# Kernel optimization log

Measured on AMD Instinct MI355X. Metric: run time of the kernel, lower is better.

Reference implementation:

```python
import jax, jax.numpy as jnp
import numpy as np

B, IN_DIM, H, OUT_DIM, T = 2048, 1024, 2048, 1024, 10


def setup_inputs() -> dict:
    key = jax.random.key(0)
    ks = jax.random.split(key, 16)
    s = lambda d: 1.0 / np.sqrt(d)
    inp = {
        "x": jax.random.normal(ks[0], (B, IN_DIM), jnp.float32),
        "z0": jax.random.normal(ks[1], (B, H), jnp.float32),
        "noise": jax.random.normal(ks[2], (T, B, H), jnp.float32),
        # input_embed: Linear(IN,H) -> SiLU -> Linear(H,H)
        "w1_in": jax.random.normal(ks[3], (IN_DIM, H), jnp.float32) * s(IN_DIM),
        "b1_in": jnp.zeros((H,), jnp.float32),
        "w2_in": jax.random.normal(ks[4], (H, H), jnp.float32) * s(H),
        "b2_in": jnp.zeros((H,), jnp.float32),
        # T blocks: Linear(2H,H) -> SiLU -> Linear(H,H), stacked over T
        "wA": jax.random.normal(ks[5], (T, 2 * H, H), jnp.float32) * s(2 * H),
        "bA": jnp.zeros((T, H), jnp.float32),
        "wB": jax.random.normal(ks[6], (T, H, H), jnp.float32) * s(H),
        "bB": jnp.zeros((T, H), jnp.float32),
        # classifier Linear(H, OUT)
        "wC": jax.random.normal(ks[7], (H, OUT_DIM), jnp.float32) * s(H),
        "bC": jnp.zeros((OUT_DIM,), jnp.float32),
    }
    return inp


def _forward(x, z0, noise, w1_in, b1_in, w2_in, b2_in, wA, bA, wB, bB, wC, bC):
    # input embedding
    h = jax.nn.silu(x @ w1_in + b1_in)
    x_embed = h @ w2_in + b2_in  # (B, H)

    alpha = jnp.linspace(0.99, 0.9, T).astype(x.dtype)          # (T,)
    noise_scale = jnp.sqrt(1.0 - alpha)                          # (T,)

    def step(z, per_t):
        wA_t, bA_t, wB_t, bB_t, n_t, a_t, ns_t = per_t
        u = jax.nn.silu(jnp.concatenate([z, x_embed], axis=-1) @ wA_t + bA_t)
        u = u @ wB_t + bB_t
        z_next = a_t * u + (1.0 - a_t) * z + ns_t * n_t
        return z_next, None

    z_final, _ = jax.lax.scan(step, z0, (wA, bA, wB, bB, noise, alpha, noise_scale))
    return z_final @ wC + bC  # (B, OUT_DIM)


def reference(x, z0, noise, w1_in, b1_in, w2_in, b2_in, wA, bA, wB, bB, wC, bC):
    return _forward(x, z0, noise, w1_in, b1_in, w2_in, b2_in, wA, bA, wB, bB, wC, bC)
```

## Files before the change

### kernel.cpp

```cpp
#include <hip/hip_runtime.h>
#include <math.h>

typedef _Float16 f16;
typedef _Float16 f16x4 __attribute__((ext_vector_type(4)));
typedef _Float16 f16x8 __attribute__((ext_vector_type(8)));
typedef float f32x4 __attribute__((ext_vector_type(4)));
typedef float fvec4 __attribute__((ext_vector_type(4)));

#define EP_SILU 0
#define EP_LIN  1
#define EP_ZUP  2
#define EP_OUT  3
#define EP_ADDP 4

struct TDesc {
  const float* W;
  f16* WT;
  long long sW, sWT;
  int R, C, nMat;
};

__device__ __forceinline__ void gll16(const void* g, void* l) {
  __builtin_amdgcn_global_load_lds((__attribute__((address_space(1))) void*)g,
                                   (__attribute__((address_space(3))) void*)l,
                                   16, 0, 0);
}

__device__ __forceinline__ void stage_tile(const f16* __restrict__ g, int ld,
                                           f16* ldsTile, int tid, int wid) {
#pragma unroll
  for (int p = 0; p < 2; ++p) {
    int row = p * 64 + (tid >> 2);
    int col = (tid & 3) * 8;
    gll16(g + (size_t)row * ld + col, ldsTile + p * 2048 + wid * 512);
  }
}

__device__ __forceinline__ void stage8(const f16* __restrict__ g, int ld,
                                       f16* ldsTile, int tid) {
  int row = tid >> 2, col = (tid & 3) * 8;
  gll16(g + (size_t)row * ld + col, ldsTile + tid * 8);
}

__device__ __forceinline__ void tpose_tile(const float* __restrict__ W,
                                           f16* __restrict__ WT, int R, int C,
                                           int r0, int c0, f16 (*t)[72],
                                           int tid) {
#pragma unroll
  for (int p = 0; p < 2; ++p) {
    int lin = p * 2048 + tid * 4;
    int r = lin >> 6, c4 = lin & 63;
    fvec4 v = *(const fvec4*)(W + (size_t)(r0 + r) * C + c0 + c4);
    t[c4 + 0][r] = (f16)v[0];
    t[c4 + 1][r] = (f16)v[1];
    t[c4 + 2][r] = (f16)v[2];
    t[c4 + 3][r] = (f16)v[3];
  }
  __syncthreads();
#pragma unroll
  for (int p = 0; p < 2; ++p) {
    int lin = p * 2048 + tid * 4;
    int c = lin >> 6, r4 = lin & 63;
    f16x4 h;
    h[0] = t[c][r4 + 0];
    h[1] = t[c][r4 + 1];
    h[2] = t[c][r4 + 2];
    h[3] = t[c][r4 + 3];
    *(f16x4*)(WT + (size_t)(c0 + c) * R + r0 + r4) = h;
  }
  __syncthreads();
}

__device__ void run_role(const TDesc d, int rid, int nr, f16 (*t)[72],
                         int tid) {
  if (d.nMat <= 0 || d.W == nullptr) return;
  int tR = d.R >> 6, tC = d.C >> 6;
  int tpm = tR * tC, tot = tpm * d.nMat;
  for (int i = rid; i < tot; i += nr) {
    int m = i / tpm, rem = i - m * tpm;
    int r0 = (rem % tR) << 6, c0 = (rem / tR) << 6;
    tpose_tile(d.W + (size_t)m * d.sW, d.WT + (size_t)m * d.sWT, d.R, d.C, r0,
               c0, t, tid);
  }
}

template <int EP>
__global__ void __launch_bounds__(512)
gemm8(const f16* __restrict__ A, int lda, const f16* __restrict__ BT, int ldb,
      int K, int N, int gx, int nbGemm, const float* __restrict__ bias,
      const f16* __restrict__ addP, f16* __restrict__ outH,
      float* __restrict__ outF, const f16* __restrict__ zOld,
      const float* __restrict__ noise, float aT, float nsT, TDesc dA,
      TDesc dB) {
  __shared__ __align__(16) char smem[65536];
  const int tid = threadIdx.x;
  const int bid = blockIdx.x;

  if (bid >= nbGemm) {
    int rid = bid - nbGemm, nr = (int)gridDim.x - nbGemm;
    f16(*t)[72] = reinterpret_cast<f16(*)[72]>(smem);
    run_role(dA, rid, nr, t, tid);
    run_role(dB, rid, nr, t, tid);
    return;
  }

  const int cpx = nbGemm >> 3;
  const int swz = (bid & 7) * cpx + (bid >> 3);
  const int by = swz / gx, bx = swz % gx;
  const int m0 = by * 128, n0 = bx * 128;

  const int lane = tid & 63, wid = tid >> 6;
  const int q = wid & 3, h = wid >> 2;
  const int wr = q >> 1, wc = q & 1;
  const int lr = lane & 15, kg = lane >> 4;

  f16* base = (f16*)smem;
  f32x4 acc[4][4] = {};

  const int nkp = K >> 6;
  auto stageAB = [&](int kp, int slot) {
    int k0 = kp << 6;
    f16* s = base + slot * 16384;
    stage8(A + (size_t)m0 * lda + k0, lda, s, tid);
    stage8(A + (size_t)m0 * lda + k0 + 32, lda, s + 4096, tid);
    stage8(BT + (size_t)n0 * ldb + k0, ldb, s + 8192, tid);
    stage8(BT + (size_t)n0 * ldb + k0 + 32, ldb, s + 12288, tid);
  };

  stageAB(0, 0);
  __syncthreads();
  int cur = 0;
  for (int kp = 0; kp < nkp; ++kp) {
    if (kp + 1 < nkp) stageAB(kp + 1, cur ^ 1);
    const f16* LA = base + cur * 16384 + h * 4096;
    const f16* LB = base + cur * 16384 + 8192 + h * 4096;
    f16x8 a[4], b[4];
#pragma unroll
    for (int m = 0; m < 4; ++m)
      a[m] = *(const f16x8*)(LA + ((wr * 64 + m * 16 + lr) * 32 + kg * 8));
#pragma unroll
    for (int n = 0; n < 4; ++n)
      b[n] = *(const f16x8*)(LB + ((wc * 64 + n * 16 + lr) * 32 + kg * 8));
#pragma unroll
    for (int m = 0; m < 4; ++m)
#pragma unroll
      for (int n = 0; n < 4; ++n)
        acc[m][n] = __builtin_amdgcn_mfma_f32_16x16x32_f16(a[m], b[n],
                                                           acc[m][n], 0, 0, 0);
    __syncthreads();
    cur ^= 1;
  }

  float* red = (float*)smem;
  if (h == 1) {
#pragma unroll
    for (int m = 0; m < 4; ++m)
#pragma unroll
      for (int n = 0; n < 4; ++n) {
        int row = wr * 64 + m * 16 + kg * 4;
        int col = wc * 64 + n * 16 + lr;
        *(f32x4*)&red[(size_t)col * 128 + row] = acc[m][n];
      }
  }
  __syncthreads();
  if (h != 0) return;

  float bcol[4];
  if constexpr (EP != EP_ADDP) {
#pragma unroll
    for (int n = 0; n < 4; ++n) bcol[n] = bias[n0 + wc * 64 + n * 16 + lr];
  }

#pragma unroll
  for (int m = 0; m < 4; ++m) {
    int rowb = m0 + wr * 64 + m * 16 + kg * 4;
    int rowl = wr * 64 + m * 16 + kg * 4;
#pragma unroll
    for (int n = 0; n < 4; ++n) {
      int col = n0 + wc * 64 + n * 16 + lr;
      int coll = wc * 64 + n * 16 + lr;
      f32x4 osum = acc[m][n] + *(const f32x4*)&red[(size_t)coll * 128 + rowl];
#pragma unroll
      for (int r = 0; r < 4; ++r) {
        size_t idx = (size_t)(rowb + r) * N + col;
        float v = osum[r];
        if constexpr (EP == EP_ADDP) v += (float)addP[idx];
        else v += bcol[n];
        if constexpr (EP == EP_SILU || EP == EP_ADDP) {
          v = v / (1.0f + __expf(-v));
          outH[idx] = (f16)v;
        } else if constexpr (EP == EP_LIN) {
          outH[idx] = (f16)v;
        } else if constexpr (EP == EP_OUT) {
          outF[idx] = v;
        } else {
          float zn = aT * v + (1.0f - aT) * (float)zOld[idx] + nsT * noise[idx];
          outH[idx] = (f16)zn;
        }
      }
    }
  }
}

template <int EP>
__global__ void __launch_bounds__(256)
gemm_bt(const f16* __restrict__ A0, const f16* __restrict__ A1, int Ksplit,
        int lda, const f16* __restrict__ BT, int ldb, long long sBT, int K,
        int N, int gx, const float* __restrict__ bias, long long sBias,
        f16* __restrict__ outH, float* __restrict__ outF, long long sOut,
        const float* __restrict__ zOld, const float* __restrict__ noise,
        float aT, float nsT) {
  __shared__ __align__(16) f16 lds[2][2][128 * 32];
  const int tid = threadIdx.x;
  const int z = blockIdx.z;
  const f16* BTz = BT + (size_t)z * sBT;
  f16* outHz = outH + (size_t)z * sOut;
  float* outFz = outF ? outF + (size_t)z * sOut : nullptr;

  const int lane = tid & 63, wid = tid >> 6;
  const int wr = wid >> 1, wc = wid & 1;
  const int lr = lane & 15, kg = lane >> 4;
  const int by = blockIdx.x / gx, bx = blockIdx.x - by * gx;
  const int m0 = by * 128, n0 = bx * 128;

  f32x4 acc[4][4] = {};
  const int nk = K >> 5;
  auto stageAB = [&](int kt, int buf) {
    int k0 = kt << 5;
    const f16* Abase = (k0 < Ksplit)
                           ? (A0 + (size_t)m0 * lda + k0)
                           : (A1 + (size_t)m0 * lda + (k0 - Ksplit));
    stage_tile(Abase, lda, &lds[buf][0][0], tid, wid);
    stage_tile(BTz + (size_t)n0 * ldb + k0, ldb, &lds[buf][1][0], tid, wid);
  };

  stageAB(0, 0);
  __syncthreads();
  int cur = 0;
  for (int kt = 0; kt < nk; ++kt) {
    if (kt + 1 < nk) stageAB(kt + 1, cur ^ 1);
    const f16* LA = &lds[cur][0][0];
    const f16* LB = &lds[cur][1][0];
    f16x8 a[4], b[4];
#pragma unroll
    for (int m = 0; m < 4; ++m)
      a[m] = *(const f16x8*)(LA + ((wr * 64 + m * 16 + lr) * 32 + kg * 8));
#pragma unroll
    for (int n = 0; n < 4; ++n)
      b[n] = *(const f16x8*)(LB + ((wc * 64 + n * 16 + lr) * 32 + kg * 8));
#pragma unroll
    for (int m = 0; m < 4; ++m)
#pragma unroll
      for (int n = 0; n < 4; ++n)
        acc[m][n] = __builtin_amdgcn_mfma_f32_16x16x32_f16(a[m], b[n],
                                                           acc[m][n], 0, 0, 0);
    __syncthreads();
    cur ^= 1;
  }

  float bcol[4];
  const float* biasz = bias + (size_t)z * sBias;
#pragma unroll
  for (int n = 0; n < 4; ++n) bcol[n] = biasz[n0 + wc * 64 + n * 16 + lr];

#pragma unroll
  for (int m = 0; m < 4; ++m) {
    int rowb = m0 + wr * 64 + m * 16 + kg * 4;
#pragma unroll
    for (int n = 0; n < 4; ++n) {
      int col = n0 + wc * 64 + n * 16 + lr;
#pragma unroll
      for (int r = 0; r < 4; ++r) {
        size_t idx = (size_t)(rowb + r) * N + col;
        float v = acc[m][n][r] + bcol[n];
        if constexpr (EP == EP_SILU) {
          v = v / (1.0f + __expf(-v));
          outHz[idx] = (f16)v;
        } else if constexpr (EP == EP_LIN) {
          outHz[idx] = (f16)v;
        } else if constexpr (EP == EP_OUT) {
          outFz[idx] = v;
        } else {
          float zn = aT * v + (1.0f - aT) * zOld[idx] + nsT * noise[idx];
          outFz[idx] = zn;
          outHz[idx] = (f16)zn;
        }
      }
    }
  }
}

__global__ void __launch_bounds__(512) tconv_role(TDesc d) {
  __shared__ __align__(16) f16 t[64][72];
  run_role(d, blockIdx.x, gridDim.x, t, threadIdx.x);
}

__global__ void __launch_bounds__(256)
cvt4(const float* __restrict__ in, f16* __restrict__ outp, int n4) {
  int i = blockIdx.x * 256 + threadIdx.x;
  if (i >= n4) return;
  fvec4 v = *(const fvec4*)(in + (size_t)i * 4);
  f16x4 h;
  h[0] = (f16)v[0];
  h[1] = (f16)v[1];
  h[2] = (f16)v[2];
  h[3] = (f16)v[3];
  *(f16x4*)(outp + (size_t)i * 4) = h;
}

__global__ void __launch_bounds__(256)
zinit4(const float* __restrict__ z0, float* __restrict__ z32,
       f16* __restrict__ z16, int n4) {
  int i = blockIdx.x * 256 + threadIdx.x;
  if (i >= n4) return;
  fvec4 v = *(const fvec4*)(z0 + (size_t)i * 4);
  *(fvec4*)(z32 + (size_t)i * 4) = v;
  f16x4 h;
  h[0] = (f16)v[0];
  h[1] = (f16)v[1];
  h[2] = (f16)v[2];
  h[3] = (f16)v[3];
  *(f16x4*)(z16 + (size_t)i * 4) = h;
}

extern "C" void kernel_launch(void* const* d_in, const int* in_sizes, int n_in,
                              void* d_out, int out_size, void* d_ws,
                              size_t ws_size, hipStream_t stream) {
  const int B = 2048, IN = 1024, H = 2048, OUT = 1024, T = 10;
  const float* x = (const float*)d_in[0];
  const float* z0 = (const float*)d_in[1];
  const float* noise = (const float*)d_in[2];
  const float* w1 = (const float*)d_in[3];
  const float* b1 = (const float*)d_in[4];
  const float* w2 = (const float*)d_in[5];
  const float* b2 = (const float*)d_in[6];
  const float* wA = (const float*)d_in[7];
  const float* bA = (const float*)d_in[8];
  const float* wB = (const float*)d_in[9];
  const float* bB = (const float*)d_in[10];
  const float* wC = (const float*)d_in[11];
  const float* bC = (const float*)d_in[12];
  float* out = (float*)d_out;

  char* ws = (char*)d_ws;
  size_t off = 0;
  auto alloc = [&](size_t bytes) {
    void* p = ws + off;
    off += (bytes + 255) & ~(size_t)255;
    return p;
  };
  TDesc none = {nullptr, nullptr, 0, 0, 0, 0, 0};

  const size_t FAST_NEED = 273000000ull;
  if (ws_size >= FAST_NEED) {
    f16* x16 = (f16*)alloc((size_t)B * IN * 2);
    f16* h16 = (f16*)alloc((size_t)B * H * 2);
    f16* xe16 = (f16*)alloc((size_t)B * H * 2);
    f16* z16 = (f16*)alloc((size_t)B * H * 2);
    f16* u16 = (f16*)alloc((size_t)B * H * 2);
    f16* p16 = (f16*)alloc((size_t)T * B * H * 2);
    f16* w1T = (f16*)alloc((size_t)IN * H * 2);
    f16* w2T = (f16*)alloc((size_t)H * H * 2);
    f16* wCT = (f16*)alloc((size_t)H * OUT * 2);
    f16* wAbotT = (f16*)alloc((size_t)T * H * H * 2);
    f16* wAtopT[2] = {(f16*)alloc((size_t)H * H * 2),
                      (f16*)alloc((size_t)H * H * 2)};
    f16* wBT2[2] = {(f16*)alloc((size_t)H * H * 2),
                    (f16*)alloc((size_t)H * H * 2)};

    cvt4<<<B * IN / 4 / 256, 256, 0, stream>>>(x, x16, B * IN / 4);
    cvt4<<<B * H / 4 / 256, 256, 0, stream>>>(z0, z16, B * H / 4);
    tconv_role<<<512, 512, 0, stream>>>(TDesc{w1, w1T, 0, 0, IN, H, 1});

    gemm8<EP_SILU><<<512, 512, 0, stream>>>(
        x16, IN, w1T, IN, IN, H, 16, 256, b1, nullptr, h16, nullptr, nullptr,
        nullptr, 0.f, 0.f, TDesc{w2, w2T, 0, 0, H, H, 1},
        TDesc{wA + (size_t)H * H, wAbotT, (long long)2 * H * H,
              (long long)H * H, H, H, 4});
    gemm8<EP_LIN><<<512, 512, 0, stream>>>(
        h16, H, w2T, H, H, H, 16, 256, b2, nullptr, xe16, nullptr, nullptr,
        nullptr, 0.f, 0.f, TDesc{wC, wCT, 0, 0, H, OUT, 1},
        TDesc{wA + (size_t)H * H + (size_t)4 * 2 * H * H,
              wAbotT + (size_t)4 * H * H, (long long)2 * H * H,
              (long long)H * H, H, H, 6});
    tconv_role<<<512, 512, 0, stream>>>(TDesc{wA, wAtopT[0], 0, 0, H, H, 1});

    gemm_bt<EP_LIN><<<dim3(256, 1, T), 256, 0, stream>>>(
        xe16, xe16, H, H, wAbotT, H, (long long)H * H, H, H, 16, bA, H, p16,
        nullptr, (long long)B * H, nullptr, nullptr, 0.f, 0.f);

    for (int t = 0; t < T; ++t) {
      float alpha = (float)(0.99 - 0.01 * (double)t);
      float ns = sqrtf(1.0f - alpha);
      gemm8<EP_ADDP><<<320, 512, 0, stream>>>(
          z16, H, wAtopT[t & 1], H, H, H, 16, 256, nullptr,
          p16 + (size_t)t * B * H, u16, nullptr, nullptr, nullptr, 0.f, 0.f,
          TDesc{wB + (size_t)t * H * H, wBT2[t & 1], 0, 0, H, H, 1}, none);
      TDesc nextA = (t < T - 1)
                        ? TDesc{wA + (size_t)(t + 1) * 2 * H * H,
                                wAtopT[(t + 1) & 1], 0, 0, H, H, 1}
                        : none;
      gemm8<EP_ZUP><<<320, 512, 0, stream>>>(
          u16, H, wBT2[t & 1], H, H, H, 16, 256, bB + (size_t)t * H, nullptr,
          z16, nullptr, z16, noise + (size_t)t * B * H, alpha, ns, nextA,
          none);
    }
    gemm8<EP_OUT><<<128, 512, 0, stream>>>(
        z16, H, wCT, H, H, OUT, 8, 128, bC, nullptr, nullptr, out, nullptr,
        nullptr, 0.f, 0.f, none, none);
  } else {
    f16* x16 = (f16*)alloc((size_t)B * IN * 2);
    f16* h16 = (f16*)alloc((size_t)B * H * 2);
    f16* xe16 = (f16*)alloc((size_t)B * H * 2);
    f16* z16 = (f16*)alloc((size_t)B * H * 2);
    f16* u16 = (f16*)alloc((size_t)B * H * 2);
    float* z32 = (float*)alloc((size_t)B * H * 4);
    f16* w1T = (f16*)alloc((size_t)IN * H * 2);
    f16* w2T = (f16*)alloc((size_t)H * H * 2);
    f16* wCT = (f16*)alloc((size_t)H * OUT * 2);
    f16* wAT = (f16*)alloc((size_t)2 * H * H * 2);
    f16* wBT = (f16*)alloc((size_t)H * H * 2);

    cvt4<<<B * IN / 4 / 256, 256, 0, stream>>>(x, x16, B * IN / 4);
    zinit4<<<B * H / 4 / 256, 256, 0, stream>>>(z0, z32, z16, B * H / 4);
    tconv_role<<<512, 512, 0, stream>>>(TDesc{w1, w1T, 0, 0, IN, H, 1});
    tconv_role<<<1024, 512, 0, stream>>>(TDesc{w2, w2T, 0, 0, H, H, 1});
    tconv_role<<<512, 512, 0, stream>>>(TDesc{wC, wCT, 0, 0, H, OUT, 1});

    gemm_bt<EP_SILU><<<dim3(256, 1, 1), 256, 0, stream>>>(
        x16, x16, IN, IN, w1T, IN, 0, IN, H, 16, b1, 0, h16, nullptr, 0,
        nullptr, nullptr, 0.f, 0.f);
    gemm_bt<EP_LIN><<<dim3(256, 1, 1), 256, 0, stream>>>(
        h16, h16, H, H, w2T, H, 0, H, H, 16, b2, 0, xe16, nullptr, 0, nullptr,
        nullptr, 0.f, 0.f);

    for (int t = 0; t < T; ++t) {
      float alpha = (float)(0.99 - 0.01 * (double)t);
      float ns = sqrtf(1.0f - alpha);
      tconv_role<<<1024, 512, 0, stream>>>(
          TDesc{wA + (size_t)t * 2 * H * H, wAT, 0, 0, 2 * H, H, 1});
      gemm_bt<EP_SILU><<<dim3(256, 1, 1), 256, 0, stream>>>(
          z16, xe16, H, H, wAT, 2 * H, 0, 2 * H, H, 16, bA + (size_t)t * H, 0,
          u16, nullptr, 0, nullptr, nullptr, 0.f, 0.f);
      tconv_role<<<1024, 512, 0, stream>>>(
          TDesc{wB + (size_t)t * H * H, wBT, 0, 0, H, H, 1});
      gemm_bt<EP_ZUP><<<dim3(256, 1, 1), 256, 0, stream>>>(
          u16, u16, H, H, wBT, H, 0, H, H, 16, bB + (size_t)t * H, 0, z16,
          z32, 0, z32, noise + (size_t)t * B * H, alpha, ns);
    }
    gemm_bt<EP_OUT><<<dim3(128, 1, 1), 256, 0, stream>>>(
        z16, z16, H, H, wCT, H, 0, H, OUT, 8, bC, 0, nullptr, out, 0, nullptr,
        nullptr, 0.f, 0.f);
  }
}
```

Measured before the change: 1.244 ms.

## Deepen gemm8 pipeline to four LDS stages and batch precompute GEMM through gemm8

```diff
diff --git a/kernel.cpp b/kernel.cpp
--- a/kernel.cpp
+++ b/kernel.cpp
@@ -84,25 +84,54 @@
   }
 }
 
+#define GEMM8_ITER(KP, VM, DO_STAGE)                                          \
+  {                                                                           \
+    asm volatile("s_waitcnt vmcnt(" #VM ")" ::: "memory");                    \
+    __builtin_amdgcn_s_barrier();                                             \
+    const int slot_ = (KP) & 3;                                               \
+    const f16* LA_ = base + slot_ * 16384 + h * 4096;                         \
+    const f16* LB_ = base + slot_ * 16384 + 8192 + h * 4096;                  \
+    f16x8 a_[4], b_[4];                                                       \
+    _Pragma("unroll") for (int m_ = 0; m_ < 4; ++m_) a_[m_] =                 \
+        *(const f16x8*)(LA_ + ((wr * 64 + m_ * 16 + lr) * 32 + kg * 8));      \
+    _Pragma("unroll") for (int n_ = 0; n_ < 4; ++n_) b_[n_] =                 \
+        *(const f16x8*)(LB_ + ((wc * 64 + n_ * 16 + lr) * 32 + kg * 8));      \
+    asm volatile("s_waitcnt lgkmcnt(0)" ::: "memory");                        \
+    __builtin_amdgcn_s_barrier();                                             \
+    if (DO_STAGE) stageAB((KP) + 3, ((KP) + 3) & 3);                          \
+    _Pragma("unroll") for (int m_ = 0; m_ < 4; ++m_)                          \
+        _Pragma("unroll") for (int n_ = 0; n_ < 4; ++n_) acc[m_][n_] =        \
+            __builtin_amdgcn_mfma_f32_16x16x32_f16(a_[m_], b_[n_],            \
+                                                   acc[m_][n_], 0, 0, 0);     \
+  }
+
 template <int EP>
 __global__ void __launch_bounds__(512)
 gemm8(const f16* __restrict__ A, int lda, const f16* __restrict__ BT, int ldb,
-      int K, int N, int gx, int nbGemm, const float* __restrict__ bias,
+      long long sBT, int K, int N, int gx, int nbGemm,
+      const float* __restrict__ bias, long long sBias,
       const f16* __restrict__ addP, f16* __restrict__ outH,
-      float* __restrict__ outF, const f16* __restrict__ zOld,
+      float* __restrict__ outF, long long sOut, const f16* __restrict__ zOld,
       const float* __restrict__ noise, float aT, float nsT, TDesc dA,
       TDesc dB) {
-  __shared__ __align__(16) char smem[65536];
+  __shared__ __align__(16) char smem[131072];
   const int tid = threadIdx.x;
   const int bid = blockIdx.x;
 
   if (bid >= nbGemm) {
-    int rid = bid - nbGemm, nr = (int)gridDim.x - nbGemm;
-    f16(*t)[72] = reinterpret_cast<f16(*)[72]>(smem);
-    run_role(dA, rid, nr, t, tid);
-    run_role(dB, rid, nr, t, tid);
+    if (blockIdx.z == 0) {
+      int rid = bid - nbGemm, nr = (int)gridDim.x - nbGemm;
+      f16(*t)[72] = reinterpret_cast<f16(*)[72]>(smem);
+      run_role(dA, rid, nr, t, tid);
+      run_role(dB, rid, nr, t, tid);
+    }
     return;
   }
+
+  const int z = blockIdx.z;
+  const f16* BTz = BT + (size_t)z * sBT;
+  f16* outHz = outH ? outH + (size_t)z * sOut : nullptr;
+  float* outFz = outF ? outF + (size_t)z * sOut : nullptr;
 
   const int cpx = nbGemm >> 3;
   const int swz = (bid & 7) * cpx + (bid >> 3);
@@ -123,33 +152,20 @@
     f16* s = base + slot * 16384;
     stage8(A + (size_t)m0 * lda + k0, lda, s, tid);
     stage8(A + (size_t)m0 * lda + k0 + 32, lda, s + 4096, tid);
-    stage8(BT + (size_t)n0 * ldb + k0, ldb, s + 8192, tid);
-    stage8(BT + (size_t)n0 * ldb + k0 + 32, ldb, s + 12288, tid);
+    stage8(BTz + (size_t)n0 * ldb + k0, ldb, s + 8192, tid);
+    stage8(BTz + (size_t)n0 * ldb + k0 + 32, ldb, s + 12288, tid);
   };
 
   stageAB(0, 0);
-  __syncthreads();
-  int cur = 0;
-  for (int kp = 0; kp < nkp; ++kp) {
-    if (kp + 1 < nkp) stageAB(kp + 1, cur ^ 1);
-    const f16* LA = base + cur * 16384 + h * 4096;
-    const f16* LB = base + cur * 16384 + 8192 + h * 4096;
-    f16x8 a[4], b[4];
-#pragma unroll
-    for (int m = 0; m < 4; ++m)
-      a[m] = *(const f16x8*)(LA + ((wr * 64 + m * 16 + lr) * 32 + kg * 8));
-#pragma unroll
-    for (int n = 0; n < 4; ++n)
-      b[n] = *(const f16x8*)(LB + ((wc * 64 + n * 16 + lr) * 32 + kg * 8));
-#pragma unroll
-    for (int m = 0; m < 4; ++m)
-#pragma unroll
-      for (int n = 0; n < 4; ++n)
-        acc[m][n] = __builtin_amdgcn_mfma_f32_16x16x32_f16(a[m], b[n],
-                                                           acc[m][n], 0, 0, 0);
-    __syncthreads();
-    cur ^= 1;
-  }
+  stageAB(1, 1);
+  stageAB(2, 2);
+  int kp = 0;
+  for (; kp + 3 < nkp; ++kp) GEMM8_ITER(kp, 8, 1);
+  GEMM8_ITER(kp, 8, 0);
+  ++kp;
+  GEMM8_ITER(kp, 4, 0);
+  ++kp;
+  GEMM8_ITER(kp, 0, 0);
 
   float* red = (float*)smem;
   if (h == 1) {
@@ -159,7 +175,7 @@
       for (int n = 0; n < 4; ++n) {
         int row = wr * 64 + m * 16 + kg * 4;
         int col = wc * 64 + n * 16 + lr;
-        *(f32x4*)&red[(size_t)col * 128 + row] = acc[m][n];
+        *(f32x4*)&red[(size_t)col * 132 + row] = acc[m][n];
       }
   }
   __syncthreads();
@@ -167,8 +183,9 @@
 
   float bcol[4];
   if constexpr (EP != EP_ADDP) {
-#pragma unroll
-    for (int n = 0; n < 4; ++n) bcol[n] = bias[n0 + wc * 64 + n * 16 + lr];
+    const float* biasz = bias + (size_t)z * sBias;
+#pragma unroll
+    for (int n = 0; n < 4; ++n) bcol[n] = biasz[n0 + wc * 64 + n * 16 + lr];
   }
 
 #pragma unroll
@@ -179,7 +196,7 @@
     for (int n = 0; n < 4; ++n) {
       int col = n0 + wc * 64 + n * 16 + lr;
       int coll = wc * 64 + n * 16 + lr;
-      f32x4 osum = acc[m][n] + *(const f32x4*)&red[(size_t)coll * 128 + rowl];
+      f32x4 osum = acc[m][n] + *(const f32x4*)&red[(size_t)coll * 132 + rowl];
 #pragma unroll
       for (int r = 0; r < 4; ++r) {
         size_t idx = (size_t)(rowb + r) * N + col;
@@ -188,14 +205,14 @@
         else v += bcol[n];
         if constexpr (EP == EP_SILU || EP == EP_ADDP) {
           v = v / (1.0f + __expf(-v));
-          outH[idx] = (f16)v;
+          outHz[idx] = (f16)v;
         } else if constexpr (EP == EP_LIN) {
-          outH[idx] = (f16)v;
+          outHz[idx] = (f16)v;
         } else if constexpr (EP == EP_OUT) {
-          outF[idx] = v;
+          outFz[idx] = v;
         } else {
           float zn = aT * v + (1.0f - aT) * (float)zOld[idx] + nsT * noise[idx];
-          outH[idx] = (f16)zn;
+          outHz[idx] = (f16)zn;
         }
       }
     }
@@ -214,7 +231,7 @@
   const int tid = threadIdx.x;
   const int z = blockIdx.z;
   const f16* BTz = BT + (size_t)z * sBT;
-  f16* outHz = outH + (size_t)z * sOut;
+  f16* outHz = outH ? outH + (size_t)z * sOut : nullptr;
   float* outFz = outF ? outF + (size_t)z * sOut : nullptr;
 
   const int lane = tid & 63, wid = tid >> 6;
@@ -373,41 +390,43 @@
     tconv_role<<<512, 512, 0, stream>>>(TDesc{w1, w1T, 0, 0, IN, H, 1});
 
     gemm8<EP_SILU><<<512, 512, 0, stream>>>(
-        x16, IN, w1T, IN, IN, H, 16, 256, b1, nullptr, h16, nullptr, nullptr,
-        nullptr, 0.f, 0.f, TDesc{w2, w2T, 0, 0, H, H, 1},
+        x16, IN, w1T, IN, 0, IN, H, 16, 256, b1, 0, nullptr, h16, nullptr, 0,
+        nullptr, nullptr, 0.f, 0.f, TDesc{w2, w2T, 0, 0, H, H, 1},
         TDesc{wA + (size_t)H * H, wAbotT, (long long)2 * H * H,
               (long long)H * H, H, H, 4});
     gemm8<EP_LIN><<<512, 512, 0, stream>>>(
-        h16, H, w2T, H, H, H, 16, 256, b2, nullptr, xe16, nullptr, nullptr,
-        nullptr, 0.f, 0.f, TDesc{wC, wCT, 0, 0, H, OUT, 1},
+        h16, H, w2T, H, 0, H, H, 16, 256, b2, 0, nullptr, xe16, nullptr, 0,
+        nullptr, nullptr, 0.f, 0.f, TDesc{wC, wCT, 0, 0, H, OUT, 1},
         TDesc{wA + (size_t)H * H + (size_t)4 * 2 * H * H,
               wAbotT + (size_t)4 * H * H, (long long)2 * H * H,
               (long long)H * H, H, H, 6});
     tconv_role<<<512, 512, 0, stream>>>(TDesc{wA, wAtopT[0], 0, 0, H, H, 1});
 
-    gemm_bt<EP_LIN><<<dim3(256, 1, T), 256, 0, stream>>>(
-        xe16, xe16, H, H, wAbotT, H, (long long)H * H, H, H, 16, bA, H, p16,
-        nullptr, (long long)B * H, nullptr, nullptr, 0.f, 0.f);
+    gemm8<EP_LIN><<<dim3(256, 1, T), 512, 0, stream>>>(
+        xe16, H, wAbotT, H, (long long)H * H, H, H, 16, 256, bA, H, nullptr,
+        p16, nullptr, (long long)B * H, nullptr, nullptr, 0.f, 0.f, none,
+        none);
 
     for (int t = 0; t < T; ++t) {
       float alpha = (float)(0.99 - 0.01 * (double)t);
       float ns = sqrtf(1.0f - alpha);
       gemm8<EP_ADDP><<<320, 512, 0, stream>>>(
-          z16, H, wAtopT[t & 1], H, H, H, 16, 256, nullptr,
-          p16 + (size_t)t * B * H, u16, nullptr, nullptr, nullptr, 0.f, 0.f,
-          TDesc{wB + (size_t)t * H * H, wBT2[t & 1], 0, 0, H, H, 1}, none);
+          z16, H, wAtopT[t & 1], H, 0, H, H, 16, 256, nullptr, 0,
+          p16 + (size_t)t * B * H, u16, nullptr, 0, nullptr, nullptr, 0.f,
+          0.f, TDesc{wB + (size_t)t * H * H, wBT2[t & 1], 0, 0, H, H, 1},
+          none);
       TDesc nextA = (t < T - 1)
                         ? TDesc{wA + (size_t)(t + 1) * 2 * H * H,
                                 wAtopT[(t + 1) & 1], 0, 0, H, H, 1}
                         : none;
       gemm8<EP_ZUP><<<320, 512, 0, stream>>>(
-          u16, H, wBT2[t & 1], H, H, H, 16, 256, bB + (size_t)t * H, nullptr,
-          z16, nullptr, z16, noise + (size_t)t * B * H, alpha, ns, nextA,
-          none);
+          u16, H, wBT2[t & 1], H, 0, H, H, 16, 256, bB + (size_t)t * H, 0,
+          nullptr, z16, nullptr, 0, z16, noise + (size_t)t * B * H, alpha, ns,
+          nextA, none);
     }
     gemm8<EP_OUT><<<128, 512, 0, stream>>>(
-        z16, H, wCT, H, H, OUT, 8, 128, bC, nullptr, nullptr, out, nullptr,
-        nullptr, 0.f, 0.f, none, none);
+        z16, H, wCT, H, 0, H, OUT, 8, 128, bC, 0, nullptr, nullptr, out, 0,
+        nullptr, nullptr, 0.f, 0.f, none, none);
   } else {
     f16* x16 = (f16*)alloc((size_t)B * IN * 2);
     f16* h16 = (f16*)alloc((size_t)B * H * 2);
```

Measured after the change: 1.330 ms. +6.9%, slower.
